# Kernel optimization log

Hardware: AMD Instinct MI355X
Metric: run time of the kernel (lower is better)

The kernel has to match this reference:

```python
import jax, jax.numpy as jnp
import numpy as np

HIDDEN = 1024
N_HEADS = 16
HEAD_DIM = HIDDEN // N_HEADS  # 64


def setup_inputs() -> dict:
    key = jax.random.key(0)
    ks = jax.random.split(key, 5)
    B, S = 4, 4096
    x = jax.random.normal(ks[0], (B, S, HIDDEN), dtype=jnp.float32)
    scale = 1.0 / np.sqrt(HIDDEN)
    wq = jax.random.normal(ks[1], (HIDDEN, HIDDEN), dtype=jnp.float32) * scale
    wk = jax.random.normal(ks[2], (HIDDEN, HIDDEN), dtype=jnp.float32) * scale
    wv = jax.random.normal(ks[3], (HIDDEN, HIDDEN), dtype=jnp.float32) * scale
    wo = jax.random.normal(ks[4], (HIDDEN, HIDDEN), dtype=jnp.float32) * scale
    return {"x": x, "wq": wq, "wk": wk, "wv": wv, "wo": wo}


def reference(x, wq, wk, wv, wo):
    # Weights stored as (out, in) like torch nn.Linear; y = x @ W^T
    B, S, H = x.shape
    q = (x @ wq.T).reshape(B, S, N_HEADS, HEAD_DIM)
    k = (x @ wk.T).reshape(B, S, N_HEADS, HEAD_DIM)
    v = (x @ wv.T).reshape(B, S, N_HEADS, HEAD_DIM)
    # Faithful to original: no transpose to (B,H,S,D) -> scores are over HEADS
    # attn: (B, S, H_heads, H_heads)
    attn = jnp.einsum("bshd,bsgd->bshg", q, k) / np.sqrt(HEAD_DIM)
    attn = jax.nn.softmax(attn, axis=-1)
    out = jnp.einsum("bshg,bsgd->bshd", attn, v).reshape(B, S, H)
    return out @ wo.T
```

## Files before the change

kernel.cpp:

```cpp
#include <hip/hip_runtime.h>
#include <hip/hip_bf16.h>


typedef __bf16 bf16;
typedef __attribute__((ext_vector_type(8))) __bf16 bf16x8;
typedef __attribute__((ext_vector_type(4))) float floatx4;

#define HIDDEN 1024
#define BM 128
#define BN 128
#define BK 32

#define FENCE() asm volatile("" ::: "memory")
#define BAR()                                                                  \
    do {                                                                       \
        FENCE();                                                               \
        __builtin_amdgcn_s_barrier();                                          \
        FENCE();                                                               \
    } while (0)
#define VMCNT(N) asm volatile("s_waitcnt vmcnt(" #N ")" ::: "memory")

__device__ __forceinline__ void async_load16(const bf16* g, bf16* lds) {
    __builtin_amdgcn_global_load_lds(
        (const __attribute__((address_space(1))) void*)g,
        (__attribute__((address_space(3))) void*)lds, 16, 0, 0);
}

__device__ __forceinline__ bf16x8 load8(const bf16* p) {
    return *(const bf16x8*)p;
}
__device__ __forceinline__ bf16x8 load8(const float* p) {
    floatx4 lo = *(const floatx4*)p;
    floatx4 hi = *(const floatx4*)(p + 4);
    bf16x8 r;
#pragma unroll
    for (int i = 0; i < 4; ++i) { r[i] = (bf16)lo[i]; r[i + 4] = (bf16)hi[i]; }
    return r;
}

__global__ __launch_bounds__(256) void cvt_all(
    const float* __restrict__ x,
    const float* __restrict__ wq, const float* __restrict__ wk,
    const float* __restrict__ wv, const float* __restrict__ wo,
    bf16* __restrict__ xb, bf16* __restrict__ wpk, int mh8)
{
    const int per = (HIDDEN * HIDDEN) / 8;
    int i = blockIdx.x * 256 + threadIdx.x;
    if (i < mh8) {
        *(bf16x8*)&xb[(size_t)i * 8] = load8(&x[(size_t)i * 8]);
    } else {
        int j = i - mh8;
        int wsel = j / per;
        int off  = (j - wsel * per) * 8;
        const float* s = wsel == 0 ? wq : wsel == 1 ? wk : wsel == 2 ? wv : wo;
        *(bf16x8*)&wpk[(size_t)j * 8] = load8(&s[off]);
    }
}


template <int S>
__device__ __forceinline__ void stage_half(const bf16* __restrict__ gbase,
                                           int ld, int kt, bf16* lhalf,
                                           int h, int tid) {
#pragma unroll
    for (int j = 0; j < 2; ++j) {
        const int ci = j * 512 + tid;
        const int rr = ci >> 3;
        const int cs = (ci & 7) ^ (rr & 7);
        const int gr = h * S + (rr & (S - 1)) + (rr >> (S == 64 ? 6 : 5)) * (2 * S);
        async_load16(&gbase[(size_t)gr * ld + kt + cs * 8], &lhalf[ci * 8]);
    }
}

__device__ __forceinline__ void ld_a4(const bf16* h, int wm, int col, int quad,
                                      int cx, bf16x8* a) {
#pragma unroll
    for (int i = 0; i < 4; ++i) {
        const int rr = i * 16 + col + (wm << 6);
#pragma unroll
        for (int kk = 0; kk < 2; ++kk)
            a[i * 2 + kk] =
                *(const bf16x8*)&h[rr * 64 + (((kk << 2) + quad) ^ cx) * 8];
    }
}
__device__ __forceinline__ void ld_b2(const bf16* h, int wn, int col, int quad,
                                      int cx, bf16x8* b) {
#pragma unroll
    for (int j = 0; j < 2; ++j) {
        const int rr = j * 16 + col + (wn << 5);
#pragma unroll
        for (int kk = 0; kk < 2; ++kk)
            b[j * 2 + kk] =
                *(const bf16x8*)&h[rr * 64 + (((kk << 2) + quad) ^ cx) * 8];
    }
}

template <int H, int G>
__device__ __forceinline__ void mmq(floatx4 (&acc)[8][4], const bf16x8 (&a)[8],
                                    const bf16x8 (&bb)[4]) {
    __builtin_amdgcn_s_setprio(1);
#pragma unroll
    for (int i = 0; i < 4; ++i)
#pragma unroll
        for (int j = 0; j < 2; ++j)
#pragma unroll
            for (int kk = 0; kk < 2; ++kk)
                acc[H * 4 + i][G * 2 + j] =
                    __builtin_amdgcn_mfma_f32_16x16x32_bf16(
                        a[i * 2 + kk], bb[j * 2 + kk],
                        acc[H * 4 + i][G * 2 + j], 0, 0, 0);
    __builtin_amdgcn_s_setprio(0);
}

template <typename TC>
__global__ __launch_bounds__(512, 2) void gemm8p(
    const bf16* __restrict__ A, const bf16* __restrict__ W,
    TC* __restrict__ C, int K, int lda, int ldc)
{
    __shared__ __align__(16) bf16 sA[2][2][128 * 64];
    __shared__ __align__(16) bf16 sB[2][2][128 * 64];

    const int tid  = threadIdx.x;
    const int lane = tid & 63;
    const int w    = tid >> 6;
    const int wm   = w >> 2;
    const int wn   = w & 3;
    const int m0   = blockIdx.x * 256;
    const int n0   = blockIdx.y * 256;
    const int col  = lane & 15;
    const int quad = lane >> 4;
    const int cx   = col & 7;

    const bf16* Ab = A + (size_t)m0 * lda;
    const bf16* Wb = W + (size_t)n0 * K;

    floatx4 acc[8][4] = {};
    bf16x8 a[8], b0[4], b1[4];

    const int T = K / 64;

    stage_half<64>(Ab, lda, 0, sA[0][0], 0, tid);
    stage_half<32>(Wb, K,   0, sB[0][0], 0, tid);
    stage_half<32>(Wb, K,   0, sB[0][1], 1, tid);
    stage_half<64>(Ab, lda, 0, sA[0][1], 1, tid);
    if (T > 1) {
        stage_half<64>(Ab, lda, 64, sA[1][0], 0, tid);
        stage_half<32>(Wb, K,   64, sB[1][0], 0, tid);
        stage_half<32>(Wb, K,   64, sB[1][1], 1, tid);
        VMCNT(6);
    } else {
        VMCNT(0);
    }
    BAR();

    for (int t = 0; t < T; ++t) {
        const int b   = t & 1;
        const int kt1 = (t + 1) * 64;
        const int kt2 = (t + 2) * 64;

        ld_a4(sA[b][0], wm, col, quad, cx, a);
        ld_b2(sB[b][0], wn, col, quad, cx, b0);
        ld_b2(sB[b][1], wn, col, quad, cx, b1);
        if (t + 1 < T) {
            stage_half<64>(Ab, lda, kt1, sA[b ^ 1][1], 1, tid);
            VMCNT(8);
        } else {
            VMCNT(0);
        }
        BAR();
        mmq<0, 0>(acc, a, b0);
        mmq<0, 1>(acc, a, b1);
        BAR();

        ld_a4(sA[b][1], wm, col, quad, cx, a);
        if (t + 2 < T) {
            stage_half<64>(Ab, lda, kt2, sA[b][0], 0, tid);
            stage_half<32>(Wb, K,   kt2, sB[b][0], 0, tid);
            stage_half<32>(Wb, K,   kt2, sB[b][1], 1, tid);
            VMCNT(8);
        } else {
            VMCNT(0);
        }
        BAR();
        mmq<1, 1>(acc, a, b1);
        mmq<1, 0>(acc, a, b0);
        BAR();
    }

#pragma unroll
    for (int mi = 0; mi < 8; ++mi) {
#pragma unroll
        for (int r = 0; r < 4; ++r) {
            const int row = m0 + wm * 128 + mi * 16 + quad * 4 + r;
#pragma unroll
            for (int ni = 0; ni < 4; ++ni) {
                const int cc = n0 + wn * 64 + ni * 16 + col;
                C[(size_t)row * ldc + cc] = (TC)acc[mi][ni][r];
            }
        }
    }
}

template <typename TA, typename TB, typename TC>
__global__ __launch_bounds__(256, 2) void gemm_bt(
    const TA* __restrict__ A, const TB* __restrict__ W,
    TC* __restrict__ C, int M, int N, int K)
{
    __shared__ __align__(16) bf16 sA[BM * BK];
    __shared__ __align__(16) bf16 sB[BN * BK];

    const int tid  = threadIdx.x;
    const int lane = tid & 63;
    const int w    = tid >> 6;
    const int wm   = w >> 1;
    const int wn   = w & 1;
    const int m0   = blockIdx.x * BM;
    const int n0   = blockIdx.y * BN;
    const int col  = lane & 15;
    const int quad = lane >> 4;

    floatx4 acc[4][4] = {};

    for (int kt = 0; kt < K; kt += BK) {
        bf16x8 ga[2], gb[2];
#pragma unroll
        for (int i = 0; i < 2; ++i) {
            const int c   = i * 256 + tid;
            const int row = c >> 2;
            const int kc  = c & 3;
            ga[i] = load8(&A[(size_t)(m0 + row) * K + kt + kc * 8]);
            gb[i] = load8(&W[(size_t)(n0 + row) * K + kt + kc * 8]);
        }
        __syncthreads();
#pragma unroll
        for (int i = 0; i < 2; ++i) {
            const int c = i * 256 + tid;
            *(bf16x8*)&sA[c * 8] = ga[i];
            *(bf16x8*)&sB[c * 8] = gb[i];
        }
        __syncthreads();

        bf16x8 af[4], bfr[4];
#pragma unroll
        for (int mi = 0; mi < 4; ++mi)
            af[mi] = *(const bf16x8*)&sA[(wm * 64 + mi * 16 + col) * BK + quad * 8];
#pragma unroll
        for (int ni = 0; ni < 4; ++ni)
            bfr[ni] = *(const bf16x8*)&sB[(wn * 64 + ni * 16 + col) * BK + quad * 8];

#pragma unroll
        for (int mi = 0; mi < 4; ++mi)
#pragma unroll
            for (int ni = 0; ni < 4; ++ni)
                acc[mi][ni] = __builtin_amdgcn_mfma_f32_16x16x32_bf16(
                    af[mi], bfr[ni], acc[mi][ni], 0, 0, 0);
    }

#pragma unroll
    for (int mi = 0; mi < 4; ++mi) {
#pragma unroll
        for (int r = 0; r < 4; ++r) {
            const int row = m0 + wm * 64 + mi * 16 + quad * 4 + r;
#pragma unroll
            for (int ni = 0; ni < 4; ++ni) {
                const int cc = n0 + wn * 64 + ni * 16 + col;
                C[(size_t)row * N + cc] = (TC)acc[mi][ni][r];
            }
        }
    }
}

__global__ __launch_bounds__(256) void attn_heads(
    bf16* base, size_t koff, size_t voff, int stride, bf16* ob)
{
    __shared__ __align__(16) bf16 sQ[4][2][3072];
    __shared__ __align__(16) bf16 sP[4][16 * 40];
    __shared__ __align__(16) bf16 sO[4][1024];

    const int tid   = threadIdx.x;
    const int lane  = tid & 63;
    const int w     = tid >> 6;
    const int col   = lane & 15;
    const int quad  = lane >> 4;
    const int t0    = blockIdx.x * 16 + w * 4;

    auto stage = [&](int tok, int s) {
        const bf16* qt = base + (size_t)tok * stride;
#pragma unroll
        for (int i = 0; i < 6; ++i) {
            const int ci = i * 64 + lane;
            const int rl = (ci >> 3) & 15;
            const int cs = (ci & 7) ^ (rl & 7);
            const bf16* src = (i < 2) ? qt : (i < 4) ? qt + koff : qt + voff;
            async_load16(&src[(rl * 8 + cs) * 8], &sQ[w][s][ci * 8]);
        }
    };

    stage(t0, 0);

#pragma unroll
    for (int it = 0; it < 4; ++it) {
        if (it < 3) stage(t0 + it + 1, (it + 1) & 1);
        if (it == 0)      { VMCNT(6);  }
        else if (it < 3)  { VMCNT(10); }
        else              { VMCNT(4);  }

        const bf16* sq = sQ[w][it & 1];
        bf16* ot = ob + (size_t)(t0 + it) * HIDDEN;

        bf16x8 qa[2], kb[2];
#pragma unroll
        for (int kk = 0; kk < 2; ++kk) {
            const int c = ((kk << 2) + quad) ^ (col & 7);
            qa[kk] = *(const bf16x8*)&sq[(col * 8 + c) * 8];
            kb[kk] = *(const bf16x8*)&sq[((16 + col) * 8 + c) * 8];
        }
        floatx4 s = {};
        s = __builtin_amdgcn_mfma_f32_16x16x32_bf16(qa[0], kb[0], s, 0, 0, 0);
        s = __builtin_amdgcn_mfma_f32_16x16x32_bf16(qa[1], kb[1], s, 0, 0, 0);

        bf16x8 va[4] = {};
        if (quad < 2) {
#pragma unroll
            for (int dt = 0; dt < 4; ++dt) {
                const int cb = dt * 2 + (col >> 3);
#pragma unroll
                for (int j = 0; j < 8; ++j) {
                    const int r = 32 + quad * 8 + j;
                    va[dt][j] = sq[(r * 8 + (cb ^ j)) * 8 + (col & 7)];
                }
            }
        }

#pragma unroll
        for (int r = 0; r < 4; ++r) {
            float e = __expf(s[r] * 0.125f);
            float su = e;
#pragma unroll
            for (int off = 1; off < 16; off <<= 1)
                su += __shfl_xor(su, off);
            sP[w][(quad * 4 + r) * 40 + col] = (bf16)(e / su);
        }

        bf16x8 pa = {};
        if (quad < 2) pa = *(const bf16x8*)&sP[w][col * 40 + quad * 8];
#pragma unroll
        for (int dt = 0; dt < 4; ++dt) {
            floatx4 o4 = {};
            o4 = __builtin_amdgcn_mfma_f32_16x16x32_bf16(va[dt], pa, o4, 0, 0, 0);
            union { bf16 h4[4]; uint2 u; } pk;
#pragma unroll
            for (int r = 0; r < 4; ++r) pk.h4[r] = (bf16)o4[r];
            const int c8 = dt * 4 + quad;
            *(uint2*)&sO[w][(col * 16 + (c8 ^ col)) * 4] = pk.u;
        }

#pragma unroll
        for (int st = 0; st < 4; ++st) {
            const int n8 = st * 64 + lane;
            const int h = n8 >> 4, c8 = n8 & 15;
            const uint2 d = *(const uint2*)&sO[w][(h * 16 + (c8 ^ h)) * 4];
            *(uint2*)&ot[n8 * 4] = d;
        }
    }
}

extern "C" void kernel_launch(void* const* d_in, const int* in_sizes, int n_in,
                              void* d_out, int out_size, void* d_ws, size_t ws_size,
                              hipStream_t stream) {
    const float* x  = (const float*)d_in[0];
    const float* wq = (const float*)d_in[1];
    const float* wk = (const float*)d_in[2];
    const float* wv = (const float*)d_in[3];
    const float* wo = (const float*)d_in[4];
    float* out = (float*)d_out;

    const int M = in_sizes[0] / HIDDEN;
    const size_t MH = (size_t)M * HIDDEN;
    const size_t WH = (size_t)HIDDEN * HIDDEN;

    const size_t need = (MH + 4 * WH + (size_t)M * 3 * HIDDEN) * sizeof(bf16);

    if (ws_size >= need && (M % 256) == 0) {
        bf16* xb  = (bf16*)d_ws;
        bf16* wpk = xb + MH;
        bf16* qkv = wpk + 4 * WH;

        const int mh8 = (int)(MH / 8);
        const int nchunks = mh8 + (int)(4 * WH / 8);
        cvt_all<<<dim3(nchunks / 256), 256, 0, stream>>>(x, wq, wk, wv, wo,
                                                         xb, wpk, mh8);

        gemm8p<bf16><<<dim3(M / 256, 3 * HIDDEN / 256), 512, 0, stream>>>(
            xb, wpk, qkv, HIDDEN, HIDDEN, 3 * HIDDEN);

        attn_heads<<<dim3(M / 16), 256, 0, stream>>>(qkv, 1024, 2048,
                                                     3 * HIDDEN, xb);

        gemm8p<float><<<dim3(M / 256, HIDDEN / 256), 512, 0, stream>>>(
            xb, wpk + 3 * WH, out, HIDDEN, HIDDEN, HIDDEN);
    } else {
        bf16* qb = (bf16*)d_ws;
        bf16* kb = qb + MH;
        bf16* vb = kb + MH;
        dim3 grid(M / BM, HIDDEN / BN), block(256);
        gemm_bt<float, float, bf16><<<grid, block, 0, stream>>>(x, wq, qb, M, HIDDEN, HIDDEN);
        gemm_bt<float, float, bf16><<<grid, block, 0, stream>>>(x, wk, kb, M, HIDDEN, HIDDEN);
        gemm_bt<float, float, bf16><<<grid, block, 0, stream>>>(x, wv, vb, M, HIDDEN, HIDDEN);
        attn_heads<<<dim3(M / 16), block, 0, stream>>>(qb, MH, 2 * MH, HIDDEN, qb);
        gemm_bt<bf16, float, float><<<grid, block, 0, stream>>>(qb, wo, out, M, HIDDEN, HIDDEN);
    }
}
```

Before: 292.3 us.

## Replace 256x256 ping-pong GEMM with smaller 256x128 tile double-buffered kernel

Replaces the 256x256-tile, BK=64 split-half ping-pong GEMM with a simpler 256x128 tile, BK=32 double-buffered kernel that uses a new XOR swizzle and allows 4 blocks per CU. Smaller per-block LDS and accumulator footprint is meant to raise occupancy and give more blocks across the grid for both the QKV and output projections. In exchange each block gets less data reuse per load, has twice as many barriers per K, and loses the interleaved half-tile scheduling.

```diff
diff --git a/kernel.cpp b/kernel.cpp
--- a/kernel.cpp
+++ b/kernel.cpp
@@ -58,140 +58,89 @@
 }
 
 
-template <int S>
-__device__ __forceinline__ void stage_half(const bf16* __restrict__ gbase,
-                                           int ld, int kt, bf16* lhalf,
-                                           int h, int tid) {
-#pragma unroll
-    for (int j = 0; j < 2; ++j) {
-        const int ci = j * 512 + tid;
-        const int rr = ci >> 3;
-        const int cs = (ci & 7) ^ (rr & 7);
-        const int gr = h * S + (rr & (S - 1)) + (rr >> (S == 64 ? 6 : 5)) * (2 * S);
-        async_load16(&gbase[(size_t)gr * ld + kt + cs * 8], &lhalf[ci * 8]);
-    }
-}
-
-__device__ __forceinline__ void ld_a4(const bf16* h, int wm, int col, int quad,
-                                      int cx, bf16x8* a) {
-#pragma unroll
-    for (int i = 0; i < 4; ++i) {
-        const int rr = i * 16 + col + (wm << 6);
-#pragma unroll
-        for (int kk = 0; kk < 2; ++kk)
-            a[i * 2 + kk] =
-                *(const bf16x8*)&h[rr * 64 + (((kk << 2) + quad) ^ cx) * 8];
-    }
-}
-__device__ __forceinline__ void ld_b2(const bf16* h, int wn, int col, int quad,
-                                      int cx, bf16x8* b) {
-#pragma unroll
-    for (int j = 0; j < 2; ++j) {
-        const int rr = j * 16 + col + (wn << 5);
-#pragma unroll
-        for (int kk = 0; kk < 2; ++kk)
-            b[j * 2 + kk] =
-                *(const bf16x8*)&h[rr * 64 + (((kk << 2) + quad) ^ cx) * 8];
-    }
-}
-
-template <int H, int G>
-__device__ __forceinline__ void mmq(floatx4 (&acc)[8][4], const bf16x8 (&a)[8],
-                                    const bf16x8 (&bb)[4]) {
-    __builtin_amdgcn_s_setprio(1);
-#pragma unroll
-    for (int i = 0; i < 4; ++i)
-#pragma unroll
-        for (int j = 0; j < 2; ++j)
-#pragma unroll
-            for (int kk = 0; kk < 2; ++kk)
-                acc[H * 4 + i][G * 2 + j] =
-                    __builtin_amdgcn_mfma_f32_16x16x32_bf16(
-                        a[i * 2 + kk], bb[j * 2 + kk],
-                        acc[H * 4 + i][G * 2 + j], 0, 0, 0);
-    __builtin_amdgcn_s_setprio(0);
+template <int NCH>
+__device__ __forceinline__ void stage_tile(const bf16* __restrict__ g, int ld,
+                                           int kt, bf16* lds, int tid) {
+#pragma unroll
+    for (int j = 0; j < NCH; ++j) {
+        const int c   = j * 512 + tid;
+        const int row = c >> 2;
+        const int kc  = (c & 3) ^ ((row >> 1) & 3);
+        async_load16(&g[(size_t)row * ld + kt + kc * 8], &lds[c * 8]);
+    }
+}
+
+__device__ __forceinline__ bf16x8 ldfrag(const bf16* buf, int base, int col,
+                                         int quad) {
+    return *(const bf16x8*)&buf[(base + col) * 32 +
+                                (quad ^ ((col >> 1) & 3)) * 8];
 }
 
 template <typename TC>
-__global__ __launch_bounds__(512, 2) void gemm8p(
+__global__ __launch_bounds__(512, 4) void gemm_oc(
     const bf16* __restrict__ A, const bf16* __restrict__ W,
     TC* __restrict__ C, int K, int lda, int ldc)
 {
-    __shared__ __align__(16) bf16 sA[2][2][128 * 64];
-    __shared__ __align__(16) bf16 sB[2][2][128 * 64];
+    __shared__ __align__(16) bf16 sA[2][256 * 32];
+    __shared__ __align__(16) bf16 sB[2][128 * 32];
 
     const int tid  = threadIdx.x;
     const int lane = tid & 63;
     const int w    = tid >> 6;
-    const int wm   = w >> 2;
-    const int wn   = w & 3;
+    const int wm   = w >> 1;
+    const int wn   = w & 1;
     const int m0   = blockIdx.x * 256;
-    const int n0   = blockIdx.y * 256;
+    const int n0   = blockIdx.y * 128;
     const int col  = lane & 15;
     const int quad = lane >> 4;
-    const int cx   = col & 7;
 
     const bf16* Ab = A + (size_t)m0 * lda;
     const bf16* Wb = W + (size_t)n0 * K;
 
-    floatx4 acc[8][4] = {};
-    bf16x8 a[8], b0[4], b1[4];
-
-    const int T = K / 64;
-
-    stage_half<64>(Ab, lda, 0, sA[0][0], 0, tid);
-    stage_half<32>(Wb, K,   0, sB[0][0], 0, tid);
-    stage_half<32>(Wb, K,   0, sB[0][1], 1, tid);
-    stage_half<64>(Ab, lda, 0, sA[0][1], 1, tid);
-    if (T > 1) {
-        stage_half<64>(Ab, lda, 64, sA[1][0], 0, tid);
-        stage_half<32>(Wb, K,   64, sB[1][0], 0, tid);
-        stage_half<32>(Wb, K,   64, sB[1][1], 1, tid);
-        VMCNT(6);
-    } else {
-        VMCNT(0);
-    }
-    BAR();
+    floatx4 acc[4][4] = {};
+
+    const int T = K / 32;
+
+    stage_tile<2>(Ab, lda, 0, sA[0], tid);
+    stage_tile<1>(Wb, K,   0, sB[0], tid);
 
     for (int t = 0; t < T; ++t) {
-        const int b   = t & 1;
-        const int kt1 = (t + 1) * 64;
-        const int kt2 = (t + 2) * 64;
-
-        ld_a4(sA[b][0], wm, col, quad, cx, a);
-        ld_b2(sB[b][0], wn, col, quad, cx, b0);
-        ld_b2(sB[b][1], wn, col, quad, cx, b1);
+        const bf16* cA = sA[t & 1];
+        const bf16* cB = sB[t & 1];
+
         if (t + 1 < T) {
-            stage_half<64>(Ab, lda, kt1, sA[b ^ 1][1], 1, tid);
-            VMCNT(8);
+            stage_tile<2>(Ab, lda, (t + 1) * 32, sA[(t + 1) & 1], tid);
+            stage_tile<1>(Wb, K,   (t + 1) * 32, sB[(t + 1) & 1], tid);
+            VMCNT(3);
         } else {
             VMCNT(0);
         }
         BAR();
-        mmq<0, 0>(acc, a, b0);
-        mmq<0, 1>(acc, a, b1);
+
+        bf16x8 a[4], b[4];
+#pragma unroll
+        for (int mi = 0; mi < 4; ++mi)
+            a[mi] = ldfrag(cA, wm * 64 + mi * 16, col, quad);
+#pragma unroll
+        for (int ni = 0; ni < 4; ++ni)
+            b[ni] = ldfrag(cB, wn * 64 + ni * 16, col, quad);
+
+        __builtin_amdgcn_s_setprio(1);
+#pragma unroll
+        for (int mi = 0; mi < 4; ++mi)
+#pragma unroll
+            for (int ni = 0; ni < 4; ++ni)
+                acc[mi][ni] = __builtin_amdgcn_mfma_f32_16x16x32_bf16(
+                    a[mi], b[ni], acc[mi][ni], 0, 0, 0);
+        __builtin_amdgcn_s_setprio(0);
         BAR();
-
-        ld_a4(sA[b][1], wm, col, quad, cx, a);
-        if (t + 2 < T) {
-            stage_half<64>(Ab, lda, kt2, sA[b][0], 0, tid);
-            stage_half<32>(Wb, K,   kt2, sB[b][0], 0, tid);
-            stage_half<32>(Wb, K,   kt2, sB[b][1], 1, tid);
-            VMCNT(8);
-        } else {
-            VMCNT(0);
-        }
-        BAR();
-        mmq<1, 1>(acc, a, b1);
-        mmq<1, 0>(acc, a, b0);
-        BAR();
-    }
-
-#pragma unroll
-    for (int mi = 0; mi < 8; ++mi) {
+    }
+
+#pragma unroll
+    for (int mi = 0; mi < 4; ++mi) {
 #pragma unroll
         for (int r = 0; r < 4; ++r) {
-            const int row = m0 + wm * 128 + mi * 16 + quad * 4 + r;
+            const int row = m0 + wm * 64 + mi * 16 + quad * 4 + r;
 #pragma unroll
             for (int ni = 0; ni < 4; ++ni) {
                 const int cc = n0 + wn * 64 + ni * 16 + col;
@@ -391,13 +340,13 @@
         cvt_all<<<dim3(nchunks / 256), 256, 0, stream>>>(x, wq, wk, wv, wo,
                                                          xb, wpk, mh8);
 
-        gemm8p<bf16><<<dim3(M / 256, 3 * HIDDEN / 256), 512, 0, stream>>>(
+        gemm_oc<bf16><<<dim3(M / 256, 3 * HIDDEN / 128), 512, 0, stream>>>(
             xb, wpk, qkv, HIDDEN, HIDDEN, 3 * HIDDEN);
 
         attn_heads<<<dim3(M / 16), 256, 0, stream>>>(qkv, 1024, 2048,
                                                      3 * HIDDEN, xb);
 
-        gemm8p<float><<<dim3(M / 256, HIDDEN / 256), 512, 0, stream>>>(
+        gemm_oc<float><<<dim3(M / 256, HIDDEN / 128), 512, 0, stream>>>(
             xb, wpk + 3 * WH, out, HIDDEN, HIDDEN, HIDDEN);
     } else {
         bf16* qb = (bf16*)d_ws;
```

After: 305.4 us. 1.05x slower.
